# Optimization experiments

Hardware: AMD Instinct MI355X
Metric: run time of the kernel (lower is better)

The kernel has to match this reference:

```python
import jax, jax.numpy as jnp
import numpy as np
from jax import lax

SCORE_THRESHOLD = 0.02
IOU_THRESHOLD = 0.5
NUM_CLASSES = 80
MAX_DETECTIONS = 10  # tf.image.non_max_suppression max_output_size in the source
ANCHORS = np.array([[1.08, 1.19], [3.42, 4.41], [6.63, 11.38], [9.42, 5.11], [16.62, 10.52]], dtype=np.float32)


def setup_inputs() -> dict:
    key = jax.random.key(0)
    k1, _ = jax.random.split(key)
    B, H, W = 16, 76, 76
    A = ANCHORS.shape[0]
    feats = jax.random.normal(k1, (B, H, W, A * (5 + NUM_CLASSES)), dtype=jnp.float32)
    anchors = jnp.asarray(ANCHORS)
    return {"feats": feats, "anchors": anchors}


def yolo_head(feats, anchors, num_classes):
    """Standard YOLOv2 decode (interpret_prediction)."""
    B, H, W, _ = feats.shape
    A = anchors.shape[0]
    feats = feats.reshape(B, H, W, A, 5 + num_classes)
    gy, gx = jnp.meshgrid(jnp.arange(H), jnp.arange(W), indexing="ij")
    grid = jnp.stack([gx, gy], axis=-1).astype(feats.dtype)  # [H,W,2] in (x,y) order
    conv_dims = jnp.array([W, H], dtype=feats.dtype)
    box_xy = (jax.nn.sigmoid(feats[..., 0:2]) + grid[None, :, :, None, :]) / conv_dims
    box_wh = jnp.exp(feats[..., 2:4]) * anchors[None, None, None, :, :] / conv_dims
    box_confidence = jax.nn.sigmoid(feats[..., 4:5])
    box_class_probs = jax.nn.softmax(feats[..., 5:], axis=-1)
    return box_xy, box_wh, box_confidence, box_class_probs


def _postprocess(feats, anchors):
    box_xy, box_wh, box_confidence, box_class_probs = yolo_head(feats, anchors, NUM_CLASSES)
    box_mins = box_xy - box_wh / 2.0
    box_maxes = box_xy + box_wh / 2.0
    # [y_min, x_min, y_max, x_max] as in the source (indices 1 then 0)
    boxes = jnp.concatenate([box_mins[..., 1:2], box_mins[..., 0:1], box_maxes[..., 1:2], box_maxes[..., 0:1]], axis=-1)
    box_scores = box_confidence * box_class_probs           # [B,H,W,A,C]
    box_classes = jnp.argmax(box_scores, axis=-1)           # [B,H,W,A]
    box_class_scores = jnp.max(box_scores, axis=-1)         # [B,H,W,A]

    # tf.boolean_mask flattens across all dims; emulate with fixed shapes by
    # marking below-threshold candidates as invalid (score -1).
    flat_boxes = boxes.reshape(-1, 4)                       # [N,4]
    flat_scores = box_class_scores.reshape(-1)              # [N]
    flat_classes = box_classes.reshape(-1)                  # [N]
    scores_work = jnp.where(flat_scores >= SCORE_THRESHOLD, flat_scores, -1.0)

    N = flat_boxes.shape[0]
    areas = jnp.maximum(flat_boxes[:, 2] - flat_boxes[:, 0], 0.0) * jnp.maximum(flat_boxes[:, 3] - flat_boxes[:, 1], 0.0)
    idx_range = jnp.arange(N)

    def step(sw, _):
        idx = jnp.argmax(sw)
        s = sw[idx]
        valid = s >= SCORE_THRESHOLD
        box = flat_boxes[idx]                               # [4] = y1,x1,y2,x2
        iy1 = jnp.maximum(box[0], flat_boxes[:, 0])
        ix1 = jnp.maximum(box[1], flat_boxes[:, 1])
        iy2 = jnp.minimum(box[2], flat_boxes[:, 2])
        ix2 = jnp.minimum(box[3], flat_boxes[:, 3])
        inter = jnp.maximum(iy2 - iy1, 0.0) * jnp.maximum(ix2 - ix1, 0.0)
        box_area = jnp.maximum(box[2] - box[0], 0.0) * jnp.maximum(box[3] - box[1], 0.0)
        iou = inter / (box_area + areas - inter + 1e-9)
        suppress = (iou > IOU_THRESHOLD) | (idx_range == idx)
        sw_new = jnp.where(valid & suppress, -1.0, sw)
        row = jnp.concatenate([box, s[None], flat_classes[idx].astype(jnp.float32)[None]])  # [6]
        row = jnp.where(valid, row, jnp.zeros_like(row))
        return sw_new, row

    _, rows = lax.scan(step, scores_work, None, length=MAX_DETECTIONS)
    return rows  # [MAX_DETECTIONS, 6] = [y1,x1,y2,x2,score,class]; zero rows are padding


def reference(feats, anchors):
    return _postprocess(feats, anchors)
```

## Files before the change

kernel.cpp:

```cpp
#include <hip/hip_runtime.h>
#include <stdint.h>

#define N_CAND 462080
#define NBINS  2048
#define HIST_BLOCKS 32
#define COMPACT_BLOCKS 64
#define TARGET 256u
#define SMAX   1024
#define SCORE_THR 0.02f
#define C_CNT 0
#define C_BIN 16
#define C_HD  32
#define C_CD  48


typedef const __attribute__((address_space(1))) uint32_t* gas1_u32;
typedef __attribute__((address_space(3))) uint32_t*       las3_u32;
#define GLOAD_LDS16(g, l) __builtin_amdgcn_global_load_lds( \
    (gas1_u32)(const void*)(g), (las3_u32)(void*)(l), 16, 0, 0)

__global__ __launch_bounds__(64) void decode_kernel(
    const float* __restrict__ feats,
    float* __restrict__ scores, unsigned char* __restrict__ cls,
    unsigned int* __restrict__ ctrl)
{
    __shared__ __align__(16) float lds[64 * 85];
    const int t = threadIdx.x;
    const long long base = (long long)blockIdx.x * 64;

    if (blockIdx.x == 0 && t == 0) { ctrl[C_HD] = 0u; ctrl[C_CD] = 0u; }

    const float4* __restrict__ src = (const float4*)(feats + base * 85);
    float4* dst = (float4*)lds;
#pragma unroll
    for (int i = 0; i < 21; ++i)
        GLOAD_LDS16(src + i * 64 + t, dst + i * 64 + t);
    if (t < 16) GLOAD_LDS16(src + 21 * 64 + t, dst + 21 * 64 + t);

    asm volatile("s_waitcnt vmcnt(0)" ::: "memory");
    __builtin_amdgcn_sched_barrier(0);

    const float* f = lds + t * 85;
    const int ci = (int)base + t;

    float m = f[5];
    int cbest = 0;
#pragma unroll
    for (int k = 1; k < 80; ++k) {
        float v = f[5 + k];
        if (v > m) { m = v; cbest = k; }
    }
    float s0 = 0.f, s1 = 0.f, s2 = 0.f, s3 = 0.f;
#pragma unroll
    for (int k = 0; k < 80; k += 4) {
        s0 += __expf(f[5 + k] - m);
        s1 += __expf(f[6 + k] - m);
        s2 += __expf(f[7 + k] - m);
        s3 += __expf(f[8 + k] - m);
    }
    float ssum = (s0 + s1) + (s2 + s3);
    float conf = 1.0f / (1.0f + __expf(-f[4]));
    float score = conf * (1.0f / ssum);

    cls[ci] = (unsigned char)cbest;
    scores[ci] = (score >= SCORE_THR) ? score : -1.0f;
}

__global__ __launch_bounds__(1024) void hist_cutoff_kernel(
    const float* __restrict__ scores, unsigned short* __restrict__ hist_part,
    unsigned int* __restrict__ ctrl)
{
    __shared__ unsigned int lh[NBINS];
    __shared__ unsigned int pa[1024], pb[1024];
    __shared__ int lastf;
    const int t = threadIdx.x;

    lh[2 * t] = 0u; lh[2 * t + 1] = 0u;
    __syncthreads();

    for (int i = blockIdx.x * 1024 + t; i < N_CAND; i += HIST_BLOCKS * 1024) {
        float s = scores[i];
        if (s >= SCORE_THR) {
            int bin = (int)(s * (float)NBINS);
            bin = bin > (NBINS - 1) ? (NBINS - 1) : bin;
            atomicAdd(&lh[bin], 1u);
        }
    }
    __syncthreads();
    unsigned int* outp = (unsigned int*)(hist_part + (size_t)blockIdx.x * NBINS);
    outp[t] = (lh[2 * t] & 0xFFFFu) | (lh[2 * t + 1] << 16);
    __syncthreads();

    if (t == 0) {
        __threadfence();
        unsigned old = atomicAdd(&ctrl[C_HD], 1u);
        lastf = (old == HIST_BLOCKS - 1) ? 1 : 0;
    }
    __syncthreads();
    if (!lastf) return;
    if (t == 0) __threadfence();
    __syncthreads();

    const unsigned int* hp32 = (const unsigned int*)hist_part;
    unsigned b0 = 0u, b1 = 0u;
#pragma unroll 4
    for (int p = 0; p < HIST_BLOCKS; ++p) {
        unsigned v = hp32[p * 1024 + t];
        b0 += v & 0xFFFFu;
        b1 += v >> 16;
    }
    lh[2 * t] = b0; lh[2 * t + 1] = b1;
    pa[t] = b0 + b1;
    __syncthreads();

    unsigned int* srcb = pa; unsigned int* dstb = pb;
    for (int off = 1; off < 1024; off <<= 1) {
        unsigned v = srcb[t] + ((t + off < 1024) ? srcb[t + off] : 0u);
        dstb[t] = v;
        __syncthreads();
        unsigned int* tmp = srcb; srcb = dstb; dstb = tmp;
    }
    unsigned St = srcb[t];
    unsigned Sn = (t < 1023) ? srcb[t + 1] : 0u;

    if (t == 0) {
        ctrl[C_CNT] = 0u;
        if (St < TARGET) ctrl[C_BIN] = 0u;
    }
    if (St >= TARGET && Sn < TARGET) {
        unsigned run = Sn + lh[2 * t + 1];
        ctrl[C_BIN] = (run >= TARGET) ? (unsigned)(2 * t + 1) : (unsigned)(2 * t);
    }
}

__device__ inline float4 decode_box(const float* __restrict__ feats,
                                    const float* __restrict__ anchors, int ci)
{
    int a = ci % 5;
    int cell = ci / 5;
    int gx = cell % 76;
    int gy = (cell / 76) % 76;
    const float* f = feats + (long long)ci * 85;
    float bx = (1.0f / (1.0f + __expf(-f[0])) + (float)gx) / 76.0f;
    float by = (1.0f / (1.0f + __expf(-f[1])) + (float)gy) / 76.0f;
    float bw = __expf(f[2]) * anchors[2 * a]     / 76.0f;
    float bh = __expf(f[3]) * anchors[2 * a + 1] / 76.0f;
    return make_float4(by - bh * 0.5f, bx - bw * 0.5f,
                       by + bh * 0.5f, bx + bw * 0.5f);
}

__global__ __launch_bounds__(1024) void compact_nms_kernel(
    const float* __restrict__ scores, unsigned int* __restrict__ ctrl,
    float* __restrict__ lscore, int* __restrict__ lidx,
    const float* __restrict__ feats, const float* __restrict__ anchors,
    const unsigned char* __restrict__ cls, float* __restrict__ out)
{
    __shared__ unsigned long long wkey[16];
    __shared__ unsigned long long bkey;
    __shared__ float4 bbox;
    __shared__ int lastf;
    const int t = threadIdx.x;

    const int cut = (int)ctrl[C_BIN];
    for (int i = blockIdx.x * 1024 + t; i < N_CAND; i += COMPACT_BLOCKS * 1024) {
        float sw = scores[i];
        if (sw >= SCORE_THR) {
            int bin = (int)(sw * (float)NBINS);
            bin = bin > (NBINS - 1) ? (NBINS - 1) : bin;
            if (bin >= cut) {
                unsigned pos = atomicAdd(&ctrl[C_CNT], 1u);
                if (pos < SMAX) { lscore[pos] = sw; lidx[pos] = i; }
            }
        }
    }
    __syncthreads();
    if (t == 0) {
        __threadfence();
        unsigned old = atomicAdd(&ctrl[C_CD], 1u);
        lastf = (old == COMPACT_BLOCKS - 1) ? 1 : 0;
    }
    __syncthreads();
    if (!lastf) return;
    if (t == 0) __threadfence();
    __syncthreads();

    unsigned cnt = ctrl[C_CNT];
    int n = (cnt < (unsigned)SMAX) ? (int)cnt : SMAX;

    unsigned long long key = 0ull;
    float4 mb = make_float4(0.f, 0.f, 0.f, 0.f);
    float  msc = 0.f, mcls = 0.f;
    unsigned midx = 0xFFFFFFFFu;
    bool aliveb = false;
    if (t < n) {
        msc  = lscore[t];
        midx = (unsigned)lidx[t];
        key  = ((unsigned long long)__float_as_uint(msc) << 32)
             | (unsigned long long)(0xFFFFFFFFu - midx);
        mb   = decode_box(feats, anchors, (int)midx);
        mcls = (float)cls[midx];
        aliveb = true;
    }

    for (int r = 0; r < 10; ++r) {
        unsigned long long k0 = aliveb ? key : 0ull;
#pragma unroll
        for (int msk = 32; msk > 0; msk >>= 1) {
            unsigned long long o = __shfl_xor(k0, msk);
            k0 = (o > k0) ? o : k0;
        }
        if ((t & 63) == 0) wkey[t >> 6] = k0;
        __syncthreads();
        if (t < 16) {
            unsigned long long v = wkey[t];
#pragma unroll
            for (int msk = 8; msk > 0; msk >>= 1) {
                unsigned long long o = __shfl_xor(v, msk);
                v = (o > v) ? o : v;
            }
            if (t == 0) bkey = v;
        }
        __syncthreads();

        unsigned long long wk = bkey;
        bool have = (wk != 0ull);
        unsigned widx = have ? (0xFFFFFFFFu - (unsigned)(wk & 0xFFFFFFFFull)) : 0xFFFFFFFFu;

        if (have && aliveb && midx == widx) {
            bbox = mb;
            out[r * 6 + 0] = mb.x;
            out[r * 6 + 1] = mb.y;
            out[r * 6 + 2] = mb.z;
            out[r * 6 + 3] = mb.w;
            out[r * 6 + 4] = msc;
            out[r * 6 + 5] = mcls;
            aliveb = false;
        }
        if (!have && t == 0) {
#pragma unroll
            for (int q = 0; q < 6; ++q) out[r * 6 + q] = 0.f;
        }
        __syncthreads();

        if (have && aliveb) {
            float4 ab = bbox;
            float aarea = fmaxf(ab.z - ab.x, 0.f) * fmaxf(ab.w - ab.y, 0.f);
            float iy1 = fmaxf(ab.x, mb.x);
            float ix1 = fmaxf(ab.y, mb.y);
            float iy2 = fminf(ab.z, mb.z);
            float ix2 = fminf(ab.w, mb.w);
            float inter = fmaxf(iy2 - iy1, 0.f) * fmaxf(ix2 - ix1, 0.f);
            float carea = fmaxf(mb.z - mb.x, 0.f) * fmaxf(mb.w - mb.y, 0.f);
            float iou = inter / (aarea + carea - inter + 1e-9f);
            if (iou > 0.5f) aliveb = false;
        }
    }
}

extern "C" void kernel_launch(void* const* d_in, const int* in_sizes, int n_in,
                              void* d_out, int out_size, void* d_ws, size_t ws_size,
                              hipStream_t stream) {
    const float* feats   = (const float*)d_in[0];
    const float* anchors = (const float*)d_in[1];
    char* ws = (char*)d_ws;

    unsigned int*   ctrl      = (unsigned int*)(ws + 0);
    unsigned short* hist_part = (unsigned short*)(ws + 256);
    float*          lscore    = (float*)(ws + 131328);
    int*            lidx      = (int*)(ws + 135424);
    float*          scores    = (float*)(ws + 139520);
    unsigned char*  cls       = (unsigned char*)(ws + 1987840);
    float*          out       = (float*)d_out;

    decode_kernel      <<<N_CAND / 64, 64, 0, stream>>>(feats, scores, cls, ctrl);
    hist_cutoff_kernel <<<HIST_BLOCKS, 1024, 0, stream>>>(scores, hist_part, ctrl);
    compact_nms_kernel <<<COMPACT_BLOCKS, 1024, 0, stream>>>(scores, ctrl, lscore, lidx,
                                                             feats, anchors, cls, out);
}
```

Measured before the change: 59.64 us.

## Double-buffer decode tiles persistently, split softmax across half-waves, defer argmax

The decode kernel becomes a persistent grid of 1792 blocks that loop over 32-candidate tiles. It double-buffers each tile into LDS with async global-to-LDS loads so the next tile's load overlaps the current tile's compute. Each candidate's 80 class logits are split between two half-waves, which combine their max and exp-sum through lane shuffles. The per-candidate class argmax and its byte store are dropped from decode and recomputed from feats only for the few surviving candidates in the NMS kernel. This lowers the per-candidate ALU and store work in the large pass, at the cost of fewer concurrent waves and some extra global reads in the serial NMS tail.

```diff
diff --git a/kernel.cpp b/kernel.cpp
--- a/kernel.cpp
+++ b/kernel.cpp
@@ -8,6 +8,10 @@
 #define TARGET 256u
 #define SMAX   1024
 #define SCORE_THR 0.02f
+#define NT 14440
+#define DGRID 1792
+#define TILEF 2720
+#define TILE4 680
 #define C_CNT 0
 #define C_BIN 16
 #define C_HD  32
@@ -19,51 +23,74 @@
 #define GLOAD_LDS16(g, l) __builtin_amdgcn_global_load_lds( \
     (gas1_u32)(const void*)(g), (las3_u32)(void*)(l), 16, 0, 0)
 
+__device__ __forceinline__ void stage_tile(const float* feats, int tile,
+                                           float* buf, int t)
+{
+    const float4* __restrict__ src = (const float4*)(feats + (size_t)tile * TILEF);
+    float4* dst = (float4*)buf;
+#pragma unroll
+    for (int i = 0; i < 10; ++i)
+        GLOAD_LDS16(src + i * 64 + t, dst + i * 64 + t);
+    if (t < 40) GLOAD_LDS16(src + 640 + t, dst + 640 + t);
+}
+
 __global__ __launch_bounds__(64) void decode_kernel(
     const float* __restrict__ feats,
-    float* __restrict__ scores, unsigned char* __restrict__ cls,
-    unsigned int* __restrict__ ctrl)
-{
-    __shared__ __align__(16) float lds[64 * 85];
+    float* __restrict__ scores, unsigned int* __restrict__ ctrl)
+{
+    __shared__ __align__(16) float lds[2 * TILEF];
     const int t = threadIdx.x;
-    const long long base = (long long)blockIdx.x * 64;
+    const int c = t & 31;
+    const int h = t >> 5;
 
     if (blockIdx.x == 0 && t == 0) { ctrl[C_HD] = 0u; ctrl[C_CD] = 0u; }
 
-    const float4* __restrict__ src = (const float4*)(feats + base * 85);
-    float4* dst = (float4*)lds;
-#pragma unroll
-    for (int i = 0; i < 21; ++i)
-        GLOAD_LDS16(src + i * 64 + t, dst + i * 64 + t);
-    if (t < 16) GLOAD_LDS16(src + 21 * 64 + t, dst + 21 * 64 + t);
-
-    asm volatile("s_waitcnt vmcnt(0)" ::: "memory");
-    __builtin_amdgcn_sched_barrier(0);
-
-    const float* f = lds + t * 85;
-    const int ci = (int)base + t;
-
-    float m = f[5];
-    int cbest = 0;
-#pragma unroll
-    for (int k = 1; k < 80; ++k) {
-        float v = f[5 + k];
-        if (v > m) { m = v; cbest = k; }
-    }
-    float s0 = 0.f, s1 = 0.f, s2 = 0.f, s3 = 0.f;
-#pragma unroll
-    for (int k = 0; k < 80; k += 4) {
-        s0 += __expf(f[5 + k] - m);
-        s1 += __expf(f[6 + k] - m);
-        s2 += __expf(f[7 + k] - m);
-        s3 += __expf(f[8 + k] - m);
-    }
-    float ssum = (s0 + s1) + (s2 + s3);
-    float conf = 1.0f / (1.0f + __expf(-f[4]));
-    float score = conf * (1.0f / ssum);
-
-    cls[ci] = (unsigned char)cbest;
-    scores[ci] = (score >= SCORE_THR) ? score : -1.0f;
+    int tile = blockIdx.x;
+    stage_tile(feats, tile, lds, t);
+    int parity = 0;
+    while (tile < NT) {
+        const int next = tile + DGRID;
+        if (next < NT) {
+            stage_tile(feats, next, lds + (parity ^ 1) * TILEF, t);
+            asm volatile("s_waitcnt vmcnt(11)" ::: "memory");
+        } else {
+            asm volatile("s_waitcnt vmcnt(0)" ::: "memory");
+        }
+        __builtin_amdgcn_sched_barrier(0);
+
+        const float* f = lds + parity * TILEF + c * 85;
+        const int kb = 5 + h * 40;
+
+        float m0 = f[kb + 0], m1 = f[kb + 1], m2 = f[kb + 2], m3 = f[kb + 3];
+#pragma unroll
+        for (int k = 4; k < 40; k += 4) {
+            m0 = fmaxf(m0, f[kb + k + 0]);
+            m1 = fmaxf(m1, f[kb + k + 1]);
+            m2 = fmaxf(m2, f[kb + k + 2]);
+            m3 = fmaxf(m3, f[kb + k + 3]);
+        }
+        float mloc = fmaxf(fmaxf(m0, m1), fmaxf(m2, m3));
+        float mall = fmaxf(mloc, __shfl_xor(mloc, 32));
+
+        float s0 = 0.f, s1 = 0.f, s2 = 0.f, s3 = 0.f;
+#pragma unroll
+        for (int k = 0; k < 40; k += 4) {
+            s0 += __expf(f[kb + k + 0] - mall);
+            s1 += __expf(f[kb + k + 1] - mall);
+            s2 += __expf(f[kb + k + 2] - mall);
+            s3 += __expf(f[kb + k + 3] - mall);
+        }
+        float sl = (s0 + s1) + (s2 + s3);
+        float sall = sl + __shfl_xor(sl, 32);
+
+        if (h == 0) {
+            float conf = 1.0f / (1.0f + __expf(-f[4]));
+            float score = conf / sall;
+            scores[tile * 32 + c] = (score >= SCORE_THR) ? score : -1.0f;
+        }
+        parity ^= 1;
+        tile = next;
+    }
 }
 
 __global__ __launch_bounds__(1024) void hist_cutoff_kernel(
@@ -153,7 +180,7 @@
     const float* __restrict__ scores, unsigned int* __restrict__ ctrl,
     float* __restrict__ lscore, int* __restrict__ lidx,
     const float* __restrict__ feats, const float* __restrict__ anchors,
-    const unsigned char* __restrict__ cls, float* __restrict__ out)
+    float* __restrict__ out)
 {
     __shared__ unsigned long long wkey[16];
     __shared__ unsigned long long bkey;
@@ -198,7 +225,14 @@
         key  = ((unsigned long long)__float_as_uint(msc) << 32)
              | (unsigned long long)(0xFFFFFFFFu - midx);
         mb   = decode_box(feats, anchors, (int)midx);
-        mcls = (float)cls[midx];
+        const float* fc = feats + (size_t)midx * 85 + 5;
+        float bm = fc[0]; int cb = 0;
+#pragma unroll 4
+        for (int k = 1; k < 80; ++k) {
+            float v = fc[k];
+            if (v > bm) { bm = v; cb = k; }
+        }
+        mcls = (float)cb;
         aliveb = true;
     }
 
@@ -269,11 +303,10 @@
     float*          lscore    = (float*)(ws + 131328);
     int*            lidx      = (int*)(ws + 135424);
     float*          scores    = (float*)(ws + 139520);
-    unsigned char*  cls       = (unsigned char*)(ws + 1987840);
     float*          out       = (float*)d_out;
 
-    decode_kernel      <<<N_CAND / 64, 64, 0, stream>>>(feats, scores, cls, ctrl);
+    decode_kernel      <<<DGRID, 64, 0, stream>>>(feats, scores, ctrl);
     hist_cutoff_kernel <<<HIST_BLOCKS, 1024, 0, stream>>>(scores, hist_part, ctrl);
     compact_nms_kernel <<<COMPACT_BLOCKS, 1024, 0, stream>>>(scores, ctrl, lscore, lidx,
-                                                             feats, anchors, cls, out);
-}
+                                                             feats, anchors, out);
+}
```

Result: slower. 71.36 us (+19.7%).
